# Kernel tuning notes

Measured on AMD Instinct MI355X. Metric: run time of the kernel, lower is better.

The kernel has to match this reference:

```python
import jax, jax.numpy as jnp
import numpy as np

GROUP = 128

def _dequant(q, s, z):
    # q: [O, K] int4 values in [0,16); s,z: [O, K//GROUP]
    O, K = q.shape
    qg = q.reshape(O, K // GROUP, GROUP)
    w = (qg - z[:, :, None]).astype(s.dtype) * s[:, :, None]
    return w.reshape(O, K)

def setup_inputs() -> dict:
    key = jax.random.key(0)
    ks = jax.random.split(key, 7)
    H, I = 4096, 14336
    x = jax.random.normal(ks[0], (2, 2048, H), jnp.float32)
    q_up = jax.random.randint(ks[1], (I, H), 0, 16, jnp.int32)
    s_up = (jax.random.uniform(ks[2], (I, H // GROUP), jnp.float32) * 0.02 + 1e-3)
    z_up = jax.random.randint(ks[3], (I, H // GROUP), 0, 16, jnp.int32)
    q_down = jax.random.randint(ks[4], (H, I), 0, 16, jnp.int32)
    s_down = (jax.random.uniform(ks[5], (H, I // GROUP), jnp.float32) * 0.02 + 1e-3)
    z_down = jax.random.randint(ks[6], (H, I // GROUP), 0, 16, jnp.int32)
    return {"x": x, "q_up": q_up, "s_up": s_up, "z_up": z_up,
            "q_down": q_down, "s_down": s_down, "z_down": z_down}

def reference(x, q_up, s_up, z_up, q_down, s_down, z_down):
    # up_proj: W4A16 dequant + GEMM, weight layout [out, in] like nn.Linear
    w_up = _dequant(q_up, s_up, z_up)        # [I, H]
    h = jnp.einsum('bsh,ih->bsi', x, w_up)   # [B, S, I]
    # NemotronH 'relu2' activation: relu(h)^2
    a = jnp.square(jax.nn.relu(h))
    w_down = _dequant(q_down, s_down, z_down)  # [H, I]
    y = jnp.einsum('bsi,hi->bsh', a, w_down)   # [B, S, H]
    return y
```

## Files before the change

kernel.cpp:

```cpp
#include <hip/hip_runtime.h>
#include <stdint.h>

typedef unsigned short u16;
typedef __attribute__((ext_vector_type(4))) float f32x4;
typedef __attribute__((ext_vector_type(8))) __bf16 bf16x8;
typedef __attribute__((ext_vector_type(8))) unsigned short u16x8;

__device__ __forceinline__ u16 f2bf(float f) {
  unsigned u = __builtin_bit_cast(unsigned, f);
  u = (u + 0x7fffu + ((u >> 16) & 1u)) >> 16;
  return (u16)u;
}

typedef __attribute__((address_space(1))) const void gvoid_t;
typedef __attribute__((address_space(3))) void lvoid_t;

__device__ __forceinline__ void gload_lds16(const void* g, void* l) {
  __builtin_amdgcn_global_load_lds((gvoid_t*)g, (lvoid_t*)l, 16, 0, 0);
}

__global__ __launch_bounds__(256)
void dequant_kernel(const int* __restrict__ q, const float* __restrict__ s,
                    const int* __restrict__ z, u16* __restrict__ w, int K) {
  const int row = blockIdx.y;
  const int k = (blockIdx.x * 256 + threadIdx.x) << 3;
  const int ng = K >> 7;
  const int g = k >> 7;
  const float sv = s[(size_t)row * ng + g];
  const float zv = (float)z[(size_t)row * ng + g];
  const int4* qp = (const int4*)(q + (size_t)row * K + k);
  const int4 a = qp[0], b = qp[1];
  u16x8 o;
  o[0] = f2bf(((float)a.x - zv) * sv);
  o[1] = f2bf(((float)a.y - zv) * sv);
  o[2] = f2bf(((float)a.z - zv) * sv);
  o[3] = f2bf(((float)a.w - zv) * sv);
  o[4] = f2bf(((float)b.x - zv) * sv);
  o[5] = f2bf(((float)b.y - zv) * sv);
  o[6] = f2bf(((float)b.z - zv) * sv);
  o[7] = f2bf(((float)b.w - zv) * sv);
  *reinterpret_cast<u16x8*>(w + (size_t)row * K + k) = o;
}

__global__ __launch_bounds__(256)
void cvt_kernel(const float* __restrict__ in, u16* __restrict__ out) {
  const size_t i = ((size_t)blockIdx.x * 256 + threadIdx.x) << 3;
  const float4* p = (const float4*)(in + i);
  const float4 a = p[0], b = p[1];
  u16x8 o;
  o[0] = f2bf(a.x); o[1] = f2bf(a.y); o[2] = f2bf(a.z); o[3] = f2bf(a.w);
  o[4] = f2bf(b.x); o[5] = f2bf(b.y); o[6] = f2bf(b.z); o[7] = f2bf(b.w);
  *reinterpret_cast<u16x8*>(out + i) = o;
}

template<bool RELU2>
__global__ __launch_bounds__(512, 2)
void gemm256(const u16* __restrict__ Ap, const u16* __restrict__ Bp,
             void* __restrict__ Cptr, int M, int N, int K) {
  __shared__ __align__(16) u16 As[2][256][64];
  __shared__ __align__(16) u16 Bs[2][256][64];
  const int tid = threadIdx.x;
  const int lane = tid & 63;
  const int wid = tid >> 6;
  const int wr = wid >> 2, wc = wid & 3;

  const int nbx = N >> 8;
  const int nwg = gridDim.x;
  int bid = blockIdx.x;
  bid = (bid & 7) * (nwg >> 3) + (bid >> 3);
  const int m0 = (bid / nbx) << 8;
  const int n0 = (bid % nbx) << 8;

  const int srow = tid >> 3;
  const int scol = tid & 7;
  const int lr = lane & 15;
  const int lk = (lane >> 4) << 3;
  const int xorc = (lr & 7) << 3;

  f32x4 acc[8][4] = {};
  bf16x8 af[8][2], bfr[4][2];

  const int nk = K >> 6;

#define STG_A(bufi, h, kt) do { _Pragma("unroll") \
  for (int l_ = 0; l_ < 2; ++l_) { \
    const int r_ = (h) * 128 + l_ * 64 + srow; \
    gload_lds16(Ap + (size_t)(m0 + r_) * K + (size_t)((kt) << 6) + ((scol ^ (srow & 7)) << 3), \
                &As[bufi][r_][scol << 3]); } } while (0)
#define STG_B(bufi, h, kt) do { _Pragma("unroll") \
  for (int l_ = 0; l_ < 2; ++l_) { \
    const int r_ = (h) * 128 + l_ * 64 + srow; \
    gload_lds16(Bp + (size_t)(n0 + r_) * K + (size_t)((kt) << 6) + ((scol ^ (srow & 7)) << 3), \
                &Bs[bufi][r_][scol << 3]); } } while (0)
#define LD_AF(bufi, i0) do { _Pragma("unroll") \
  for (int i_ = 0; i_ < 4; ++i_) { _Pragma("unroll") \
    for (int ks_ = 0; ks_ < 2; ++ks_) \
      af[(i0) + i_][ks_] = *reinterpret_cast<const bf16x8*>( \
        &As[bufi][wr * 128 + ((i0) + i_) * 16 + lr][(ks_ * 32 + lk) ^ xorc]); } } while (0)
#define LD_BF(bufi, j0) do { _Pragma("unroll") \
  for (int j_ = 0; j_ < 2; ++j_) { _Pragma("unroll") \
    for (int ks_ = 0; ks_ < 2; ++ks_) \
      bfr[(j0) + j_][ks_] = *reinterpret_cast<const bf16x8*>( \
        &Bs[bufi][wc * 64 + ((j0) + j_) * 16 + lr][(ks_ * 32 + lk) ^ xorc]); } } while (0)
#define MFMA_Q(I0, J0) do { _Pragma("unroll") \
  for (int ks_ = 0; ks_ < 2; ++ks_) { _Pragma("unroll") \
    for (int i_ = 0; i_ < 4; ++i_) { _Pragma("unroll") \
      for (int j_ = 0; j_ < 2; ++j_) \
        acc[(I0) + i_][(J0) + j_] = __builtin_amdgcn_mfma_f32_16x16x32_bf16( \
          af[(I0) + i_][ks_], bfr[(J0) + j_][ks_], acc[(I0) + i_][(J0) + j_], 0, 0, 0); } } } while (0)
#define BARRIER() do { asm volatile("" ::: "memory"); __builtin_amdgcn_s_barrier(); \
  asm volatile("" ::: "memory"); } while (0)
#define PH_TAIL(Q) do { BARRIER(); \
  asm volatile("s_waitcnt lgkmcnt(0)" ::: "memory"); \
  __builtin_amdgcn_s_setprio(1); Q; __builtin_amdgcn_s_setprio(0); \
  BARRIER(); } while (0)
#define PH_TAIL_VM(Q) do { BARRIER(); \
  asm volatile("s_waitcnt lgkmcnt(0)" ::: "memory"); \
  __builtin_amdgcn_s_setprio(1); Q; __builtin_amdgcn_s_setprio(0); \
  asm volatile("s_waitcnt vmcnt(4)" ::: "memory"); \
  BARRIER(); } while (0)

  STG_A(0, 0, 0); STG_A(0, 1, 0);
  STG_B(0, 0, 0); STG_B(0, 1, 0);
  STG_A(1, 0, 1); STG_A(1, 1, 1);
  asm volatile("s_waitcnt vmcnt(4)" ::: "memory");
  BARRIER();

  const int nit = nk >> 1;
  for (int it = 0; it < nit; ++it) {
    const int t1 = it * 2 + 1;
    int ta2 = it * 2 + 2; if (ta2 >= nk) ta2 -= nk;
    int ta3 = it * 2 + 3; if (ta3 >= nk) ta3 -= nk;
    LD_AF(0, 0); LD_BF(0, 0);
    STG_B(1, 0, t1);
    PH_TAIL(MFMA_Q(0, 0));
    LD_AF(0, 4);
    STG_B(1, 1, t1);
    PH_TAIL(MFMA_Q(4, 0));
    LD_BF(0, 2);
    STG_A(0, 0, ta2);
    PH_TAIL(MFMA_Q(4, 2));
    STG_A(0, 1, ta2);
    PH_TAIL_VM(MFMA_Q(0, 2));
    LD_AF(1, 0); LD_BF(1, 0);
    STG_B(0, 0, ta2);
    PH_TAIL(MFMA_Q(0, 0));
    LD_AF(1, 4);
    STG_B(0, 1, ta2);
    PH_TAIL(MFMA_Q(4, 0));
    LD_BF(1, 2);
    STG_A(1, 0, ta3);
    PH_TAIL(MFMA_Q(4, 2));
    STG_A(1, 1, ta3);
    PH_TAIL_VM(MFMA_Q(0, 2));
  }
  asm volatile("s_waitcnt vmcnt(0)" ::: "memory");

  const int crow = (lane >> 4) << 2;
  const int ccol = lane & 15;
#pragma unroll
  for (int i = 0; i < 8; ++i) {
#pragma unroll
    for (int j = 0; j < 4; ++j) {
#pragma unroll
      for (int q = 0; q < 4; ++q) {
        const int m = m0 + wr * 128 + i * 16 + crow + q;
        const int n = n0 + wc * 64 + j * 16 + ccol;
        const float v = acc[i][j][q];
        if constexpr (RELU2) {
          const float r = fmaxf(v, 0.f);
          ((u16*)Cptr)[(size_t)m * N + n] = f2bf(r * r);
        } else {
          ((float*)Cptr)[(size_t)m * N + n] = v;
        }
      }
    }
  }
#undef STG_A
#undef STG_B
#undef LD_AF
#undef LD_BF
#undef MFMA_Q
#undef BARRIER
#undef PH_TAIL
#undef PH_TAIL_VM
}

extern "C" void kernel_launch(void* const* d_in, const int* in_sizes, int n_in,
                              void* d_out, int out_size, void* d_ws, size_t ws_size,
                              hipStream_t stream) {
  const float* x    = (const float*)d_in[0];
  const int*   q_up = (const int*)d_in[1];
  const float* s_up = (const float*)d_in[2];
  const int*   z_up = (const int*)d_in[3];
  const int*   q_dn = (const int*)d_in[4];
  const float* s_dn = (const float*)d_in[5];
  const int*   z_dn = (const int*)d_in[6];
  float* y = (float*)d_out;

  const int H = 4096, I = 14336;
  const int M = in_sizes[0] / H;

  const size_t wbytes = (size_t)I * H * 2;
  const size_t abytes = (size_t)M * I * 2;
  const size_t xbytes = (size_t)M * H * 2;
  u16* wbuf = (u16*)d_ws;
  u16* abuf = (u16*)((char*)d_ws + wbytes);
  u16* xbf  = (u16*)((char*)d_ws + wbytes + abytes);
  if (ws_size < wbytes + abytes + xbytes) return;

  dequant_kernel<<<dim3(H / 8 / 256, I), 256, 0, stream>>>(q_up, s_up, z_up, wbuf, H);
  cvt_kernel<<<dim3((int)(((size_t)M * H) >> 11)), 256, 0, stream>>>(x, xbf);
  gemm256<true><<<dim3((M / 256) * (I / 256)), 512, 0, stream>>>(xbf, wbuf, abuf, M, I, H);
  dequant_kernel<<<dim3(I / 8 / 256, H), 256, 0, stream>>>(q_dn, s_dn, z_dn, wbuf, I);
  gemm256<false><<<dim3((M / 256) * (H / 256)), 512, 0, stream>>>(abuf, wbuf, y, M, H, I);
}
```

Before: 1.094 ms.

## Restructure GEMM main loop into per-k-slice phases with full-tile prefetch

```diff
diff --git a/kernel.cpp b/kernel.cpp
--- a/kernel.cpp
+++ b/kernel.cpp
@@ -78,7 +78,7 @@
   const int xorc = (lr & 7) << 3;
 
   f32x4 acc[8][4] = {};
-  bf16x8 af[8][2], bfr[4][2];
+  bf16x8 a1[4], a2[4], a3[4], a4[4], b1[4], b2[4];
 
   const int nk = K >> 6;
 
@@ -92,69 +92,47 @@
     const int r_ = (h) * 128 + l_ * 64 + srow; \
     gload_lds16(Bp + (size_t)(n0 + r_) * K + (size_t)((kt) << 6) + ((scol ^ (srow & 7)) << 3), \
                 &Bs[bufi][r_][scol << 3]); } } while (0)
-#define LD_AF(bufi, i0) do { _Pragma("unroll") \
+#define RD_A(bufi, ks, half, dst) do { _Pragma("unroll") \
+  for (int i_ = 0; i_ < 4; ++i_) { \
+    const int row_ = wr * 128 + ((half) * 4 + i_) * 16 + lr; \
+    dst[i_] = *reinterpret_cast<const bf16x8*>(&As[bufi][row_][((ks) * 32 + lk) ^ xorc]); } } while (0)
+#define RD_B(bufi, ks, dst) do { _Pragma("unroll") \
+  for (int j_ = 0; j_ < 4; ++j_) { \
+    const int row_ = wc * 64 + j_ * 16 + lr; \
+    dst[j_] = *reinterpret_cast<const bf16x8*>(&Bs[bufi][row_][((ks) * 32 + lk) ^ xorc]); } } while (0)
+#define MFMA16(ASET, BSET, I0) do { _Pragma("unroll") \
   for (int i_ = 0; i_ < 4; ++i_) { _Pragma("unroll") \
-    for (int ks_ = 0; ks_ < 2; ++ks_) \
-      af[(i0) + i_][ks_] = *reinterpret_cast<const bf16x8*>( \
-        &As[bufi][wr * 128 + ((i0) + i_) * 16 + lr][(ks_ * 32 + lk) ^ xorc]); } } while (0)
-#define LD_BF(bufi, j0) do { _Pragma("unroll") \
-  for (int j_ = 0; j_ < 2; ++j_) { _Pragma("unroll") \
-    for (int ks_ = 0; ks_ < 2; ++ks_) \
-      bfr[(j0) + j_][ks_] = *reinterpret_cast<const bf16x8*>( \
-        &Bs[bufi][wc * 64 + ((j0) + j_) * 16 + lr][(ks_ * 32 + lk) ^ xorc]); } } while (0)
-#define MFMA_Q(I0, J0) do { _Pragma("unroll") \
-  for (int ks_ = 0; ks_ < 2; ++ks_) { _Pragma("unroll") \
-    for (int i_ = 0; i_ < 4; ++i_) { _Pragma("unroll") \
-      for (int j_ = 0; j_ < 2; ++j_) \
-        acc[(I0) + i_][(J0) + j_] = __builtin_amdgcn_mfma_f32_16x16x32_bf16( \
-          af[(I0) + i_][ks_], bfr[(J0) + j_][ks_], acc[(I0) + i_][(J0) + j_], 0, 0, 0); } } } while (0)
-#define BARRIER() do { asm volatile("" ::: "memory"); __builtin_amdgcn_s_barrier(); \
+    for (int j_ = 0; j_ < 4; ++j_) \
+      acc[(I0) + i_][j_] = __builtin_amdgcn_mfma_f32_16x16x32_bf16( \
+        ASET[i_], BSET[j_], acc[(I0) + i_][j_], 0, 0, 0); } } while (0)
+#define BAR() do { asm volatile("" ::: "memory"); __builtin_amdgcn_s_barrier(); \
   asm volatile("" ::: "memory"); } while (0)
-#define PH_TAIL(Q) do { BARRIER(); \
-  asm volatile("s_waitcnt lgkmcnt(0)" ::: "memory"); \
-  __builtin_amdgcn_s_setprio(1); Q; __builtin_amdgcn_s_setprio(0); \
-  BARRIER(); } while (0)
-#define PH_TAIL_VM(Q) do { BARRIER(); \
-  asm volatile("s_waitcnt lgkmcnt(0)" ::: "memory"); \
-  __builtin_amdgcn_s_setprio(1); Q; __builtin_amdgcn_s_setprio(0); \
-  asm volatile("s_waitcnt vmcnt(4)" ::: "memory"); \
-  BARRIER(); } while (0)
+#define VMGATE() asm volatile("s_waitcnt vmcnt(0)" ::: "memory")
+#define TILE(p, q, ktn) do { \
+  RD_B(p, 0, b1); RD_A(p, 0, 0, a1); RD_A(p, 0, 1, a2); \
+  STG_A(q, 0, ktn); STG_A(q, 1, ktn); \
+  BAR(); __builtin_amdgcn_s_setprio(1); MFMA16(a1, b1, 0); __builtin_amdgcn_s_setprio(0); BAR(); \
+  RD_A(p, 1, 0, a3); RD_B(p, 1, b2); \
+  STG_B(q, 0, ktn); STG_B(q, 1, ktn); \
+  BAR(); __builtin_amdgcn_s_setprio(1); MFMA16(a2, b1, 4); __builtin_amdgcn_s_setprio(0); BAR(); \
+  RD_A(p, 1, 1, a4); \
+  BAR(); __builtin_amdgcn_s_setprio(1); MFMA16(a3, b2, 0); __builtin_amdgcn_s_setprio(0); BAR(); \
+  VMGATE(); \
+  BAR(); __builtin_amdgcn_s_setprio(1); MFMA16(a4, b2, 4); __builtin_amdgcn_s_setprio(0); BAR(); \
+} while (0)
 
   STG_A(0, 0, 0); STG_A(0, 1, 0);
   STG_B(0, 0, 0); STG_B(0, 1, 0);
-  STG_A(1, 0, 1); STG_A(1, 1, 1);
-  asm volatile("s_waitcnt vmcnt(4)" ::: "memory");
-  BARRIER();
+  VMGATE();
+  BAR();
 
   const int nit = nk >> 1;
   for (int it = 0; it < nit; ++it) {
-    const int t1 = it * 2 + 1;
-    int ta2 = it * 2 + 2; if (ta2 >= nk) ta2 -= nk;
-    int ta3 = it * 2 + 3; if (ta3 >= nk) ta3 -= nk;
-    LD_AF(0, 0); LD_BF(0, 0);
-    STG_B(1, 0, t1);
-    PH_TAIL(MFMA_Q(0, 0));
-    LD_AF(0, 4);
-    STG_B(1, 1, t1);
-    PH_TAIL(MFMA_Q(4, 0));
-    LD_BF(0, 2);
-    STG_A(0, 0, ta2);
-    PH_TAIL(MFMA_Q(4, 2));
-    STG_A(0, 1, ta2);
-    PH_TAIL_VM(MFMA_Q(0, 2));
-    LD_AF(1, 0); LD_BF(1, 0);
-    STG_B(0, 0, ta2);
-    PH_TAIL(MFMA_Q(0, 0));
-    LD_AF(1, 4);
-    STG_B(0, 1, ta2);
-    PH_TAIL(MFMA_Q(4, 0));
-    LD_BF(1, 2);
-    STG_A(1, 0, ta3);
-    PH_TAIL(MFMA_Q(4, 2));
-    STG_A(1, 1, ta3);
-    PH_TAIL_VM(MFMA_Q(0, 2));
+    const int t1 = 2 * it + 1;
+    int t2 = 2 * it + 2; if (t2 >= nk) t2 = 0;
+    TILE(0, 1, t1);
+    TILE(1, 0, t2);
   }
-  asm volatile("s_waitcnt vmcnt(0)" ::: "memory");
 
   const int crow = (lane >> 4) << 2;
   const int ccol = lane & 15;
@@ -178,12 +156,12 @@
   }
 #undef STG_A
 #undef STG_B
-#undef LD_AF
-#undef LD_BF
-#undef MFMA_Q
-#undef BARRIER
-#undef PH_TAIL
-#undef PH_TAIL_VM
+#undef RD_A
+#undef RD_B
+#undef MFMA16
+#undef BAR
+#undef VMGATE
+#undef TILE
 }
 
 extern "C" void kernel_launch(void* const* d_in, const int* in_sizes, int n_in,
```

New measurement: 1.068 ms. 2.3% less time.
